# Optimization experiments

Hardware: AMD Instinct MI355X
Metric: run time of the kernel (lower is better)

The kernel has to match this reference:

```python
import jax, jax.numpy as jnp
import numpy as np

B, T_INIT, IN, H, OUT, GEN = 128, 50, 171, 1024, 171, 100


def setup_inputs() -> dict:
    key = jax.random.key(0)
    ks = jax.random.split(key, 20)
    s = 1.0 / np.sqrt(H)  # torch LSTMCell/Linear init scale

    def u(k, shape):
        return jax.random.uniform(k, shape, jnp.float32, -s, s)

    return {
        "initial_seq": jax.random.normal(ks[0], (B, T_INIT, IN), jnp.float32),
        "generate_frames_number": GEN,
        "w_ih1": u(ks[1], (4 * H, IN)), "w_hh1": u(ks[2], (4 * H, H)),
        "b_ih1": u(ks[3], (4 * H,)), "b_hh1": u(ks[4], (4 * H,)),
        "w_ih2": u(ks[5], (4 * H, H)), "w_hh2": u(ks[6], (4 * H, H)),
        "b_ih2": u(ks[7], (4 * H,)), "b_hh2": u(ks[8], (4 * H,)),
        "w_ih3": u(ks[9], (4 * H, H)), "w_hh3": u(ks[10], (4 * H, H)),
        "b_ih3": u(ks[11], (4 * H,)), "b_hh3": u(ks[12], (4 * H,)),
        "w_dec": u(ks[13], (OUT, H)), "b_dec": u(ks[14], (OUT,)),
    }


def _lstm_cell(x, h, c, w_ih, w_hh, b_ih, b_hh):
    # PyTorch LSTMCell: gates ordered (i, f, g, o)
    gates = x @ w_ih.T + b_ih + h @ w_hh.T + b_hh
    i, f, g, o = jnp.split(gates, 4, axis=-1)
    c_new = jax.nn.sigmoid(f) * c + jax.nn.sigmoid(i) * jnp.tanh(g)
    h_new = jax.nn.sigmoid(o) * jnp.tanh(c_new)
    return h_new, c_new


def reference(initial_seq, generate_frames_number,
              w_ih1, w_hh1, b_ih1, b_hh1,
              w_ih2, w_hh2, b_ih2, b_hh2,
              w_ih3, w_hh3, b_ih3, b_hh3,
              w_dec, b_dec):
    batch = initial_seq.shape[0]
    hid = w_hh1.shape[1]
    z = jnp.zeros((batch, hid), initial_seq.dtype)

    def step(carry, in_frame):
        h0, c0, h1, c1, h2, c2 = carry
        h0, c0 = _lstm_cell(in_frame, h0, c0, w_ih1, w_hh1, b_ih1, b_hh1)
        h1, c1 = _lstm_cell(h0, h1, c1, w_ih2, w_hh2, b_ih2, b_hh2)
        h2, c2 = _lstm_cell(h1, h2, c2, w_ih3, w_hh3, b_ih3, b_hh3)
        out = h2 @ w_dec.T + b_dec
        return (h0, c0, h1, c1, h2, c2), out

    # Conditioning phase: feed ground-truth frames; only states (and last out) matter.
    carry = (z, z, z, z, z, z)
    def cond_step(cs, frame):
        carry, _ = cs
        carry, out = step(carry, frame)
        return (carry, out), None
    (carry, current_frame), _ = jax.lax.scan(
        cond_step, (carry, jnp.zeros((batch, w_dec.shape[0]), initial_seq.dtype)),
        jnp.swapaxes(initial_seq, 0, 1))  # [T_init, B, IN]

    def gen_step(cs, _):
        carry, frame = cs
        carry, out = step(carry, frame)
        return (carry, out), out
    _, outs = jax.lax.scan(gen_step, (carry, current_frame), None,
                           length=generate_frames_number)
    return jnp.swapaxes(outs, 0, 1)  # [B, GEN, OUT]
```

## Files before the change

### kernel.cpp

```cpp
#include <hip/hip_runtime.h>

typedef __attribute__((ext_vector_type(8))) short short8;
typedef __attribute__((ext_vector_type(8))) _Float16 f16x8;
typedef __attribute__((ext_vector_type(4))) float f32x4;

#define GENF 100
#define TCOND 50
#define BATCH 128
#define HID 1024
#define INP 171
#define INPAD 192
#define OUTN 171
#define OUTPAD 176
#define SPLITS 4
#define TILES 64

static __device__ __forceinline__ unsigned short f2h(float f) {
  _Float16 h = (_Float16)f;
  return __builtin_bit_cast(unsigned short, h);
}
static __device__ __forceinline__ float h2f(unsigned short s) {
  return (float)__builtin_bit_cast(_Float16, s);
}
static __device__ __forceinline__ f16x8 ld8(const unsigned short* p) {
  short8 v = *reinterpret_cast<const short8*>(p);
  return __builtin_bit_cast(f16x8, v);
}
static __device__ __forceinline__ float sigm(float x) { return 1.f / (1.f + __expf(-x)); }

__global__ __launch_bounds__(256) void lstm_gemm_k(
    const unsigned short* __restrict__ xh_, const unsigned short* __restrict__ xl_,
    int ldx, int xc,
    const unsigned short* __restrict__ hh_, const unsigned short* __restrict__ hl_,
    const unsigned short* __restrict__ wH,
    int ldw, int NK,
    const float* __restrict__ bias,
    float* __restrict__ c,
    unsigned short* __restrict__ ohh, unsigned short* __restrict__ ohl,
    float* __restrict__ partials, unsigned* __restrict__ counters)
{
  __shared__ __align__(16) char smem[98304];
  const int t = threadIdx.x;
  const int lane = t & 63, wv = t >> 6;
  const int nt = blockIdx.x & (TILES - 1), sp = blockIdx.x >> 6;
  const int n0 = nt * 64 + wv * 16;
  const int nit = NK / SPLITS;
  const int beg = sp * nit;
  const int ns = nit >> 1;

  const int r_row = lane & 15, kg = lane >> 4;
  const int rslot = kg ^ (r_row & 3);
  const int srow = t >> 2;
  const size_t bcol = (size_t)(n0 + r_row) * ldw + kg * 8;

  auto stage1 = [&](char* dst, int ck) {
    const unsigned short *sh, *sl;
    int ld, k0;
    if (ck < xc) { sh = xh_; sl = xl_; ld = ldx; k0 = ck * 32; }
    else { sh = hh_; sl = hl_; ld = HID; k0 = (ck - xc) * 32; }
#pragma unroll
    for (int j = 0; j < 2; ++j) {
      int rowp = j * 64 + srow;
      int slot = (t & 3) ^ (rowp & 3);
      const unsigned short* gh = sh + (size_t)rowp * ld + k0 + slot * 8;
      const unsigned short* gl = sl + (size_t)rowp * ld + k0 + slot * 8;
      char* dh = dst + j * 4096 + wv * 1024;
      char* dl = dst + 8192 + j * 4096 + wv * 1024;
      __builtin_amdgcn_global_load_lds((const __attribute__((address_space(1))) void*)gh,
                                       (__attribute__((address_space(3))) void*)dh, 16, 0, 0);
      __builtin_amdgcn_global_load_lds((const __attribute__((address_space(1))) void*)gl,
                                       (__attribute__((address_space(3))) void*)dl, 16, 0, 0);
    }
  };

  f32x4 zz = {0.f, 0.f, 0.f, 0.f};
  f32x4 acc[8] = {zz, zz, zz, zz, zz, zz, zz, zz};

  char* bA = smem;
  char* bB = smem + 32768;
  char* bC = smem + 65536;

  stage1(bA, beg);
  stage1(bA + 16384, beg + 1);
  f16x8 b0h0 = ld8(wH + bcol + (size_t)(beg + 0) * 32);
  f16x8 b0h1 = ld8(wH + bcol + (size_t)(beg + 1) * 32);
  __builtin_amdgcn_sched_barrier(0);
  stage1(bB, beg + 2);
  stage1(bB + 16384, beg + 3);
  f16x8 b1h0 = ld8(wH + bcol + (size_t)(beg + 2) * 32);
  f16x8 b1h1 = ld8(wH + bcol + (size_t)(beg + 3) * 32);
  __builtin_amdgcn_sched_barrier(0);

  for (int i = 0; i < ns; ++i) {
    int ck = beg + 2 * i + 4;
    if (ck >= beg + nit) ck = beg;
    stage1(bC, ck);
    stage1(bC + 16384, ck + 1);
    f16x8 b2h0 = ld8(wH + bcol + (size_t)ck * 32);
    f16x8 b2h1 = ld8(wH + bcol + (size_t)(ck + 1) * 32);
    __builtin_amdgcn_sched_barrier(0);

    asm volatile("s_waitcnt vmcnt(20)" ::: "memory");
    __builtin_amdgcn_s_barrier();
    __builtin_amdgcn_sched_barrier(0);

#pragma unroll
    for (int ch = 0; ch < 2; ++ch) {
      f16x8 ah[8], al[8];
#pragma unroll
      for (int rg = 0; rg < 8; ++rg) {
        int ro = ch * 16384 + (rg * 16 + r_row) * 64 + rslot * 16;
        ah[rg] = *reinterpret_cast<const f16x8*>(bA + ro);
        al[rg] = *reinterpret_cast<const f16x8*>(bA + ro + 8192);
      }
      f16x8 BH = ch ? b0h1 : b0h0;
#pragma unroll
      for (int rg = 0; rg < 8; ++rg)
        acc[rg] = __builtin_amdgcn_mfma_f32_16x16x32_f16(ah[rg], BH, acc[rg], 0, 0, 0);
#pragma unroll
      for (int rg = 0; rg < 8; ++rg)
        acc[rg] = __builtin_amdgcn_mfma_f32_16x16x32_f16(al[rg], BH, acc[rg], 0, 0, 0);
    }
    __builtin_amdgcn_sched_barrier(0);
    __builtin_amdgcn_s_barrier();

    char* tmp = bA; bA = bB; bB = bC; bC = tmp;
    b0h0 = b1h0; b0h1 = b1h1;
    b1h0 = b2h0; b1h1 = b2h1;
  }

  {
    float* pb = partials + (size_t)sp * (BATCH * 4096);
    const int cn = n0 + r_row;
    const int mb = kg * 4;
#pragma unroll
    for (int rg = 0; rg < 8; ++rg)
#pragma unroll
      for (int r = 0; r < 4; ++r)
        pb[(size_t)(rg * 16 + mb + r) * 4096 + cn] = acc[rg][r];
  }

  __syncthreads();
  __shared__ unsigned oldv;
  if (t == 0)
    oldv = __hip_atomic_fetch_add(&counters[nt], 1u, __ATOMIC_ACQ_REL, __HIP_MEMORY_SCOPE_AGENT);
  __syncthreads();
  if (oldv != SPLITS - 1) return;

  (void)__hip_atomic_load(&counters[nt], __ATOMIC_ACQUIRE, __HIP_MEMORY_SCOPE_AGENT);
  const int fc = t & 15, fm = t >> 4;
  const int nh = nt * 16 + fc;
  const f32x4 bv = *reinterpret_cast<const f32x4*>(&bias[nh * 4]);
#pragma unroll
  for (int p = 0; p < 8; ++p) {
    int m = fm + p * 16;
    size_t gi0 = (size_t)m * 4096 + nh * 4;
    f32x4 s = *reinterpret_cast<const f32x4*>(&partials[gi0]);
#pragma unroll
    for (int q = 1; q < SPLITS; ++q)
      s += *reinterpret_cast<const f32x4*>(&partials[gi0 + (size_t)q * BATCH * 4096]);
    float gi = sigm(s[0] + bv[0]);
    float gf = sigm(s[1] + bv[1]);
    float gg = tanhf(s[2] + bv[2]);
    float go = sigm(s[3] + bv[3]);
    size_t sidx = (size_t)m * HID + nh;
    float cn2 = gf * c[sidx] + gi * gg;
    c[sidx] = cn2;
    float h = go * tanhf(cn2);
    unsigned short h16 = f2h(h);
    ohh[sidx] = h16;
    ohl[sidx] = f2h(h - h2f(h16));
  }
  __syncthreads();
  if (t == 0)
    __hip_atomic_store(&counters[nt], 0u, __ATOMIC_RELAXED, __HIP_MEMORY_SCOPE_AGENT);
}

__global__ __launch_bounds__(256) void dec_k(
    const unsigned short* __restrict__ hhi, const unsigned short* __restrict__ hlo,
    const unsigned short* __restrict__ wdh,
    const float* __restrict__ bd,
    float* __restrict__ outp,
    unsigned short* __restrict__ fxhi, unsigned short* __restrict__ fxlo)
{
  const int wave = threadIdx.x >> 6, lane = threadIdx.x & 63;
  const int n0 = ((int)blockIdx.x % 11) * 16;
  const int m0 = ((int)blockIdx.x / 11) * 16;
  const int row = lane & 15, kg = lane >> 4;
  f32x4 acc = {0.f, 0.f, 0.f, 0.f};
  const unsigned short* pah = hhi + (size_t)(m0 + row) * HID + kg * 8 + wave * 256;
  const unsigned short* pal = hlo + (size_t)(m0 + row) * HID + kg * 8 + wave * 256;
  const unsigned short* pbh = wdh + (size_t)(n0 + row) * HID + kg * 8 + wave * 256;
#pragma unroll
  for (int kk = 0; kk < 8; ++kk) {
    int off = kk * 32;
    f16x8 a1 = ld8(pah + off), a2 = ld8(pal + off);
    f16x8 b1 = ld8(pbh + off);
    acc = __builtin_amdgcn_mfma_f32_16x16x32_f16(a1, b1, acc, 0, 0, 0);
    acc = __builtin_amdgcn_mfma_f32_16x16x32_f16(a2, b1, acc, 0, 0, 0);
  }
  __shared__ f32x4 red[4][64];
  if (wave) red[wave][lane] = acc;
  __syncthreads();
  if (wave == 0) {
    acc += red[1][lane];
    acc += red[2][lane];
    acc += red[3][lane];
    const int col = lane & 15, rg = lane >> 4;
#pragma unroll
    for (int r = 0; r < 4; ++r) {
      int m = m0 + rg * 4 + r;
      int n = n0 + col;
      if (n < OUTN) {
        float v = acc[r] + bd[n];
        if (outp) outp[(size_t)m * (GENF * OUTN) + n] = v;
        unsigned short vh = f2h(v);
        fxhi[(size_t)m * INPAD + n] = vh;
        fxlo[(size_t)m * INPAD + n] = f2h(v - h2f(vh));
      }
    }
  }
}

__global__ void cvt_w_k(const float* __restrict__ src, unsigned short* __restrict__ w16,
                        int C, int Cpad, int co, int dstride)
{
  int idx = blockIdx.x * 256 + threadIdx.x;
  if (idx >= 4096 * Cpad) return;
  int r = idx / Cpad, cc = idx - r * Cpad;
  float v = (cc < C) ? src[(size_t)r * C + cc] : 0.f;
  int rp = (r & 1023) * 4 + (r >> 10);
  w16[(size_t)rp * dstride + co + cc] = f2h(v);
}

__global__ void cvt_wd_k(const float* __restrict__ src, unsigned short* __restrict__ w16,
                         int R, int C, int Rp, int Cp)
{
  int idx = blockIdx.x * 256 + threadIdx.x;
  if (idx >= Rp * Cp) return;
  int r = idx / Cp, c2 = idx - r * Cp;
  float v = (r < R && c2 < C) ? src[(size_t)r * C + c2] : 0.f;
  w16[idx] = f2h(v);
}

__global__ void bias_perm_k(const float* __restrict__ a, const float* __restrict__ b,
                            float* __restrict__ dst)
{
  int i = blockIdx.x * 256 + threadIdx.x;
  if (i < 4096) dst[(i & 1023) * 4 + (i >> 10)] = a[i] + b[i];
}

__global__ void biaspad_k(const float* __restrict__ a, float* __restrict__ dst, int n, int np)
{
  int i = blockIdx.x * 256 + threadIdx.x;
  if (i < np) dst[i] = (i < n) ? a[i] : 0.f;
}

__global__ void xcond_k(const float* __restrict__ seq, unsigned short* __restrict__ xhi,
                        unsigned short* __restrict__ xlo)
{
  int idx = blockIdx.x * 256 + threadIdx.x;
  const int total = TCOND * BATCH * INPAD;
  if (idx >= total) return;
  int t = idx / (BATCH * INPAD);
  int rem = idx - t * (BATCH * INPAD);
  int b = rem / INPAD;
  int k = rem - b * INPAD;
  float v = (k < INP) ? seq[((size_t)b * TCOND + t) * INP + k] : 0.f;
  unsigned short h = f2h(v);
  xhi[idx] = h;
  xlo[idx] = f2h(v - h2f(h));
}

extern "C" void kernel_launch(void* const* d_in, const int* in_sizes, int n_in,
                              void* d_out, int out_size, void* d_ws, size_t ws_size,
                              hipStream_t stream)
{
  (void)in_sizes; (void)n_in; (void)out_size;
  const float* seq   = (const float*)d_in[0];
  const float* w_ih1 = (const float*)d_in[2];
  const float* w_hh1 = (const float*)d_in[3];
  const float* b_ih1 = (const float*)d_in[4];
  const float* b_hh1 = (const float*)d_in[5];
  const float* w_ih2 = (const float*)d_in[6];
  const float* w_hh2 = (const float*)d_in[7];
  const float* b_ih2 = (const float*)d_in[8];
  const float* b_hh2 = (const float*)d_in[9];
  const float* w_ih3 = (const float*)d_in[10];
  const float* w_hh3 = (const float*)d_in[11];
  const float* b_ih3 = (const float*)d_in[12];
  const float* b_hh3 = (const float*)d_in[13];
  const float* w_dec = (const float*)d_in[14];
  const float* b_dec = (const float*)d_in[15];
  float* out = (float*)d_out;

  char* ws = (char*)d_ws;
  size_t off = 0;
  auto alloc = [&](size_t bytes) -> char* {
    off = (off + 255) & ~(size_t)255;
    char* p = ws + off;
    off += bytes;
    return p;
  };
  auto us = [&](size_t n) { return (unsigned short*)alloc(n * 2); };
  auto fl = [&](size_t n) { return (float*)alloc(n * 4); };

  const int K1P = 1280;
  const int K2 = 2 * HID;
  unsigned short *W1 = us((size_t)4096 * K1P);
  unsigned short *W2 = us((size_t)4096 * K2);
  unsigned short *W3 = us((size_t)4096 * K2);
  unsigned short *wd = us((size_t)OUTPAD * HID);
  float *b1 = fl(4096), *b2 = fl(4096), *b3 = fl(4096), *bd = fl(OUTPAD);
  unsigned short *xch = us((size_t)TCOND * BATCH * INPAD), *xcl = us((size_t)TCOND * BATCH * INPAD);
  float* partials = fl((size_t)SPLITS * BATCH * 4096);

  size_t state_beg = (off + 255) & ~(size_t)255;
  float *c0 = fl((size_t)BATCH * HID), *c1 = fl((size_t)BATCH * HID), *c2 = fl((size_t)BATCH * HID);
  unsigned short* Hh[3][2];
  unsigned short* Hl[3][2];
  for (int L = 0; L < 3; ++L)
    for (int p = 0; p < 2; ++p) {
      Hh[L][p] = us((size_t)BATCH * HID);
      Hl[L][p] = us((size_t)BATCH * HID);
    }
  unsigned short *fxh = us((size_t)BATCH * INPAD), *fxl = us((size_t)BATCH * INPAD);
  unsigned* counters = (unsigned*)alloc(TILES * 4);
  size_t state_end = off;

  if (off > ws_size) return;

  hipMemsetAsync(ws + state_beg, 0, state_end - state_beg, stream);
  hipMemsetAsync(W1, 0, (size_t)4096 * K1P * 2, stream);

  auto cw = [&](const float* s, unsigned short* w, int C, int Cpad, int co, int ds2) {
    int n = 4096 * Cpad;
    cvt_w_k<<<(n + 255) / 256, 256, 0, stream>>>(s, w, C, Cpad, co, ds2);
  };
  cw(w_ih1, W1, INP, INPAD, 0, K1P);
  cw(w_hh1, W1, HID, HID, INPAD, K1P);
  cw(w_ih2, W2, HID, HID, 0, K2);
  cw(w_hh2, W2, HID, HID, HID, K2);
  cw(w_ih3, W3, HID, HID, 0, K2);
  cw(w_hh3, W3, HID, HID, HID, K2);
  {
    int n = OUTPAD * HID;
    cvt_wd_k<<<(n + 255) / 256, 256, 0, stream>>>(w_dec, wd, OUTN, HID, OUTPAD, HID);
  }
  bias_perm_k<<<16, 256, 0, stream>>>(b_ih1, b_hh1, b1);
  bias_perm_k<<<16, 256, 0, stream>>>(b_ih2, b_hh2, b2);
  bias_perm_k<<<16, 256, 0, stream>>>(b_ih3, b_hh3, b3);
  biaspad_k<<<1, 256, 0, stream>>>(b_dec, bd, OUTN, OUTPAD);
  {
    int n = TCOND * BATCH * INPAD;
    xcond_k<<<(n + 255) / 256, 256, 0, stream>>>(seq, xch, xcl);
  }

  for (int s = 0; s < TCOND + GENF; ++s) {
    const unsigned short *xh, *xl;
    if (s < TCOND) {
      xh = xch + (size_t)s * BATCH * INPAD;
      xl = xcl + (size_t)s * BATCH * INPAD;
    } else {
      xh = fxh;
      xl = fxl;
    }
    int pp = s & 1, np = pp ^ 1;
    lstm_gemm_k<<<TILES * SPLITS, 256, 0, stream>>>(xh, xl, INPAD, INPAD / 32,
        Hh[0][pp], Hl[0][pp], W1, K1P, K1P / 32, b1, c0,
        Hh[0][np], Hl[0][np], partials, counters);
    lstm_gemm_k<<<TILES * SPLITS, 256, 0, stream>>>(Hh[0][np], Hl[0][np], HID, HID / 32,
        Hh[1][pp], Hl[1][pp], W2, K2, K2 / 32, b2, c1,
        Hh[1][np], Hl[1][np], partials, counters);
    lstm_gemm_k<<<TILES * SPLITS, 256, 0, stream>>>(Hh[1][np], Hl[1][np], HID, HID / 32,
        Hh[2][pp], Hl[2][pp], W3, K2, K2 / 32, b3, c2,
        Hh[2][np], Hl[2][np], partials, counters);
    if (s == TCOND - 1) {
      dec_k<<<88, 256, 0, stream>>>(Hh[2][np], Hl[2][np], wd, bd,
                                    (float*)nullptr, fxh, fxl);
    } else if (s >= TCOND) {
      dec_k<<<88, 256, 0, stream>>>(Hh[2][np], Hl[2][np], wd, bd,
                                    out + (size_t)(s - TCOND) * OUTN, fxh, fxl);
    }
  }
}
```

Before: 14.10 ms.

## Fuse all timesteps into one persistent kernel with global phase barriers

Replaces about 550 separate kernel launches (three LSTM layers plus the decoder per step) with a single persistent kernel of 256 blocks. Blocks run every step and layer in a loop and synchronize through an atomic phase counter with spin-waits. This removes launch overhead and inter-kernel gaps on the serial recurrence. The cost is a grid-wide barrier after each phase, and it relies on all 256 blocks being co-resident, otherwise it deadlocks.

```diff
diff --git a/kernel.cpp b/kernel.cpp
--- a/kernel.cpp
+++ b/kernel.cpp
@@ -14,6 +14,7 @@
 #define OUTPAD 176
 #define SPLITS 4
 #define TILES 64
+#define NBLK 256
 
 static __device__ __forceinline__ unsigned short f2h(float f) {
   _Float16 h = (_Float16)f;
@@ -28,7 +29,32 @@
 }
 static __device__ __forceinline__ float sigm(float x) { return 1.f / (1.f + __expf(-x)); }
 
-__global__ __launch_bounds__(256) void lstm_gemm_k(
+static __device__ __forceinline__ void wait_phase(unsigned* ctr, unsigned tgt) {
+  __syncthreads();
+  if (threadIdx.x == 0) {
+    while (__hip_atomic_load(ctr, __ATOMIC_RELAXED, __HIP_MEMORY_SCOPE_AGENT) < tgt)
+      __builtin_amdgcn_s_sleep(4);
+    (void)__hip_atomic_load(ctr, __ATOMIC_ACQUIRE, __HIP_MEMORY_SCOPE_AGENT);
+  }
+  __syncthreads();
+}
+
+struct Params {
+  const unsigned short* xch; const unsigned short* xcl;
+  unsigned short* fxh; unsigned short* fxl;
+  const unsigned short* wH[3];
+  const float* bias[3];
+  float* c[3];
+  unsigned short* hh[3][2]; unsigned short* hl[3][2];
+  const unsigned short* wd; const float* bd;
+  float* out;
+  float* partials;
+  unsigned* counters;
+  unsigned* phase_ctr;
+};
+
+static __device__ __forceinline__ void layer_phase(
+    char* smem, int blk,
     const unsigned short* __restrict__ xh_, const unsigned short* __restrict__ xl_,
     int ldx, int xc,
     const unsigned short* __restrict__ hh_, const unsigned short* __restrict__ hl_,
@@ -37,12 +63,12 @@
     const float* __restrict__ bias,
     float* __restrict__ c,
     unsigned short* __restrict__ ohh, unsigned short* __restrict__ ohl,
-    float* __restrict__ partials, unsigned* __restrict__ counters)
-{
-  __shared__ __align__(16) char smem[98304];
+    float* __restrict__ partials, unsigned* __restrict__ counters,
+    unsigned* __restrict__ phase_ctr)
+{
   const int t = threadIdx.x;
   const int lane = t & 63, wv = t >> 6;
-  const int nt = blockIdx.x & (TILES - 1), sp = blockIdx.x >> 6;
+  const int nt = blk & (TILES - 1), sp = blk >> 6;
   const int n0 = nt * 64 + wv * 16;
   const int nit = NK / SPLITS;
   const int beg = sp * nit;
@@ -172,34 +198,37 @@
     ohl[sidx] = f2h(h - h2f(h16));
   }
   __syncthreads();
-  if (t == 0)
+  if (t == 0) {
     __hip_atomic_store(&counters[nt], 0u, __ATOMIC_RELAXED, __HIP_MEMORY_SCOPE_AGENT);
-}
-
-__global__ __launch_bounds__(256) void dec_k(
+    __hip_atomic_fetch_add(phase_ctr, 1u, __ATOMIC_RELEASE, __HIP_MEMORY_SCOPE_AGENT);
+  }
+}
+
+static __device__ __forceinline__ void dec_phase(
+    char* smem, int blk,
     const unsigned short* __restrict__ hhi, const unsigned short* __restrict__ hlo,
-    const unsigned short* __restrict__ wdh,
-    const float* __restrict__ bd,
-    float* __restrict__ outp,
-    unsigned short* __restrict__ fxhi, unsigned short* __restrict__ fxlo)
+    const unsigned short* __restrict__ wd,
+    const float* __restrict__ bd, float* __restrict__ outp,
+    unsigned short* __restrict__ fxhi, unsigned short* __restrict__ fxlo,
+    unsigned* __restrict__ phase_ctr)
 {
   const int wave = threadIdx.x >> 6, lane = threadIdx.x & 63;
-  const int n0 = ((int)blockIdx.x % 11) * 16;
-  const int m0 = ((int)blockIdx.x / 11) * 16;
+  const int n0 = (blk % 11) * 16;
+  const int m0 = (blk / 11) * 16;
   const int row = lane & 15, kg = lane >> 4;
   f32x4 acc = {0.f, 0.f, 0.f, 0.f};
   const unsigned short* pah = hhi + (size_t)(m0 + row) * HID + kg * 8 + wave * 256;
   const unsigned short* pal = hlo + (size_t)(m0 + row) * HID + kg * 8 + wave * 256;
-  const unsigned short* pbh = wdh + (size_t)(n0 + row) * HID + kg * 8 + wave * 256;
+  const unsigned short* pbh = wd + (size_t)(n0 + row) * HID + kg * 8 + wave * 256;
 #pragma unroll
   for (int kk = 0; kk < 8; ++kk) {
-    int off = kk * 32;
-    f16x8 a1 = ld8(pah + off), a2 = ld8(pal + off);
-    f16x8 b1 = ld8(pbh + off);
+    int off2 = kk * 32;
+    f16x8 a1 = ld8(pah + off2), a2 = ld8(pal + off2);
+    f16x8 b1 = ld8(pbh + off2);
     acc = __builtin_amdgcn_mfma_f32_16x16x32_f16(a1, b1, acc, 0, 0, 0);
     acc = __builtin_amdgcn_mfma_f32_16x16x32_f16(a2, b1, acc, 0, 0, 0);
   }
-  __shared__ f32x4 red[4][64];
+  f32x4 (*red)[64] = (f32x4(*)[64])smem;
   if (wave) red[wave][lane] = acc;
   __syncthreads();
   if (wave == 0) {
@@ -218,6 +247,49 @@
         fxhi[(size_t)m * INPAD + n] = vh;
         fxlo[(size_t)m * INPAD + n] = f2h(v - h2f(vh));
       }
+    }
+  }
+  __syncthreads();
+  if (threadIdx.x == 0)
+    __hip_atomic_fetch_add(phase_ctr, 1u, __ATOMIC_RELEASE, __HIP_MEMORY_SCOPE_AGENT);
+}
+
+__global__ __launch_bounds__(256) void lstm_persist_k(Params p) {
+  __shared__ __align__(16) char smem[98304];
+  const int blk = blockIdx.x;
+  unsigned tgt = 0;
+  for (int s = 0; s < TCOND + GENF; ++s) {
+    const int pp = s & 1, np = pp ^ 1;
+    for (int L = 0; L < 3; ++L) {
+      const unsigned short *xh, *xl;
+      int ldx, xc, ldw, NK;
+      if (L == 0) {
+        if (s < TCOND) {
+          xh = p.xch + (size_t)s * BATCH * INPAD;
+          xl = p.xcl + (size_t)s * BATCH * INPAD;
+        } else {
+          xh = p.fxh;
+          xl = p.fxl;
+        }
+        ldx = INPAD; xc = INPAD / 32; ldw = 1280; NK = 40;
+      } else {
+        xh = p.hh[L - 1][np]; xl = p.hl[L - 1][np];
+        ldx = HID; xc = HID / 32; ldw = 2 * HID; NK = 64;
+      }
+      layer_phase(smem, blk, xh, xl, ldx, xc, p.hh[L][pp], p.hl[L][pp],
+                  p.wH[L], ldw, NK, p.bias[L], p.c[L],
+                  p.hh[L][np], p.hl[L][np], p.partials, p.counters, p.phase_ctr);
+      tgt += TILES;
+      wait_phase(p.phase_ctr, tgt);
+    }
+    if (s >= TCOND - 1) {
+      if (blk < 88) {
+        float* outp = (s >= TCOND) ? p.out + (size_t)(s - TCOND) * OUTN : (float*)0;
+        dec_phase(smem, blk, p.hh[2][np], p.hl[2][np], p.wd, p.bd,
+                  outp, p.fxh, p.fxl, p.phase_ctr);
+      }
+      tgt += 88;
+      wait_phase(p.phase_ctr, tgt);
     }
   }
 }
@@ -326,6 +398,7 @@
     }
   unsigned short *fxh = us((size_t)BATCH * INPAD), *fxl = us((size_t)BATCH * INPAD);
   unsigned* counters = (unsigned*)alloc(TILES * 4);
+  unsigned* phase_ctr = (unsigned*)alloc(4);
   size_t state_end = off;
 
   if (off > ws_size) return;
@@ -356,31 +429,20 @@
     xcond_k<<<(n + 255) / 256, 256, 0, stream>>>(seq, xch, xcl);
   }
 
-  for (int s = 0; s < TCOND + GENF; ++s) {
-    const unsigned short *xh, *xl;
-    if (s < TCOND) {
-      xh = xch + (size_t)s * BATCH * INPAD;
-      xl = xcl + (size_t)s * BATCH * INPAD;
-    } else {
-      xh = fxh;
-      xl = fxl;
-    }
-    int pp = s & 1, np = pp ^ 1;
-    lstm_gemm_k<<<TILES * SPLITS, 256, 0, stream>>>(xh, xl, INPAD, INPAD / 32,
-        Hh[0][pp], Hl[0][pp], W1, K1P, K1P / 32, b1, c0,
-        Hh[0][np], Hl[0][np], partials, counters);
-    lstm_gemm_k<<<TILES * SPLITS, 256, 0, stream>>>(Hh[0][np], Hl[0][np], HID, HID / 32,
-        Hh[1][pp], Hl[1][pp], W2, K2, K2 / 32, b2, c1,
-        Hh[1][np], Hl[1][np], partials, counters);
-    lstm_gemm_k<<<TILES * SPLITS, 256, 0, stream>>>(Hh[1][np], Hl[1][np], HID, HID / 32,
-        Hh[2][pp], Hl[2][pp], W3, K2, K2 / 32, b3, c2,
-        Hh[2][np], Hl[2][np], partials, counters);
-    if (s == TCOND - 1) {
-      dec_k<<<88, 256, 0, stream>>>(Hh[2][np], Hl[2][np], wd, bd,
-                                    (float*)nullptr, fxh, fxl);
-    } else if (s >= TCOND) {
-      dec_k<<<88, 256, 0, stream>>>(Hh[2][np], Hl[2][np], wd, bd,
-                                    out + (size_t)(s - TCOND) * OUTN, fxh, fxl);
-    }
-  }
-}
+  Params P;
+  P.xch = xch; P.xcl = xcl; P.fxh = fxh; P.fxl = fxl;
+  P.wH[0] = W1; P.wH[1] = W2; P.wH[2] = W3;
+  P.bias[0] = b1; P.bias[1] = b2; P.bias[2] = b3;
+  P.c[0] = c0; P.c[1] = c1; P.c[2] = c2;
+  for (int L = 0; L < 3; ++L)
+    for (int p2 = 0; p2 < 2; ++p2) {
+      P.hh[L][p2] = Hh[L][p2];
+      P.hl[L][p2] = Hl[L][p2];
+    }
+  P.wd = wd; P.bd = bd;
+  P.out = out;
+  P.partials = partials;
+  P.counters = counters;
+  P.phase_ctr = phase_ctr;
+  lstm_persist_k<<<NBLK, 256, 0, stream>>>(P);
+}
```

New measurement: 18.89 ms. 1.34x slower.

## Drop split-K partials; each block computes full K for 16 gate columns

Applied to the files above, without the earlier changes.

Replaces the split-K scheme (64 N-tiles × 4 K-splits, fp32 partials written to global memory, atomic counter, last-block reduction) with 256 blocks that each own 16 gate columns across the full K range and all 128 batch rows. The LSTM cell epilogue reads the accumulators through shared memory instead of global partials, which removes the partial-sum traffic and the atomic synchronisation. In exchange, each block runs a K loop four times longer with fewer MFMAs per staged A tile, and every block re-stages the whole activation matrix into LDS, so LDS and L2 pressure rise. Padding allocations are added after the layer-0 state buffers, apparently so the K-loop prefetch wrap does not read past the buffer.

```diff
diff --git a/kernel.cpp b/kernel.cpp
--- a/kernel.cpp
+++ b/kernel.cpp
@@ -12,8 +12,6 @@
 #define INPAD 192
 #define OUTN 171
 #define OUTPAD 176
-#define SPLITS 4
-#define TILES 64
 
 static __device__ __forceinline__ unsigned short f2h(float f) {
   _Float16 h = (_Float16)f;
@@ -36,22 +34,19 @@
     int ldw, int NK,
     const float* __restrict__ bias,
     float* __restrict__ c,
-    unsigned short* __restrict__ ohh, unsigned short* __restrict__ ohl,
-    float* __restrict__ partials, unsigned* __restrict__ counters)
+    unsigned short* __restrict__ ohh, unsigned short* __restrict__ ohl)
 {
   __shared__ __align__(16) char smem[98304];
   const int t = threadIdx.x;
   const int lane = t & 63, wv = t >> 6;
-  const int nt = blockIdx.x & (TILES - 1), sp = blockIdx.x >> 6;
-  const int n0 = nt * 64 + wv * 16;
-  const int nit = NK / SPLITS;
-  const int beg = sp * nit;
-  const int ns = nit >> 1;
+  const int blk = blockIdx.x;
+  const int ns = NK >> 1;
 
   const int r_row = lane & 15, kg = lane >> 4;
   const int rslot = kg ^ (r_row & 3);
   const int srow = t >> 2;
-  const size_t bcol = (size_t)(n0 + r_row) * ldw + kg * 8;
+  const size_t bcol = (size_t)(blk * 16 + r_row) * ldw + kg * 8;
+  const int arow = wv * 32;
 
   auto stage1 = [&](char* dst, int ck) {
     const unsigned short *sh, *sl;
@@ -74,26 +69,26 @@
   };
 
   f32x4 zz = {0.f, 0.f, 0.f, 0.f};
-  f32x4 acc[8] = {zz, zz, zz, zz, zz, zz, zz, zz};
+  f32x4 acc0 = zz, acc1 = zz;
 
   char* bA = smem;
   char* bB = smem + 32768;
   char* bC = smem + 65536;
 
-  stage1(bA, beg);
-  stage1(bA + 16384, beg + 1);
-  f16x8 b0h0 = ld8(wH + bcol + (size_t)(beg + 0) * 32);
-  f16x8 b0h1 = ld8(wH + bcol + (size_t)(beg + 1) * 32);
+  stage1(bA, 0);
+  stage1(bA + 16384, 1);
+  f16x8 b0h0 = ld8(wH + bcol + (size_t)0 * 32);
+  f16x8 b0h1 = ld8(wH + bcol + (size_t)1 * 32);
   __builtin_amdgcn_sched_barrier(0);
-  stage1(bB, beg + 2);
-  stage1(bB + 16384, beg + 3);
-  f16x8 b1h0 = ld8(wH + bcol + (size_t)(beg + 2) * 32);
-  f16x8 b1h1 = ld8(wH + bcol + (size_t)(beg + 3) * 32);
+  stage1(bB, 2);
+  stage1(bB + 16384, 3);
+  f16x8 b1h0 = ld8(wH + bcol + (size_t)2 * 32);
+  f16x8 b1h1 = ld8(wH + bcol + (size_t)3 * 32);
   __builtin_amdgcn_sched_barrier(0);
 
   for (int i = 0; i < ns; ++i) {
-    int ck = beg + 2 * i + 4;
-    if (ck >= beg + nit) ck = beg;
+    int ck = 2 * i + 4;
+    if (ck >= NK) ck = 0;
     stage1(bC, ck);
     stage1(bC + 16384, ck + 1);
     f16x8 b2h0 = ld8(wH + bcol + (size_t)ck * 32);
@@ -106,20 +101,16 @@
 
 #pragma unroll
     for (int ch = 0; ch < 2; ++ch) {
-      f16x8 ah[8], al[8];
-#pragma unroll
-      for (int rg = 0; rg < 8; ++rg) {
-        int ro = ch * 16384 + (rg * 16 + r_row) * 64 + rslot * 16;
-        ah[rg] = *reinterpret_cast<const f16x8*>(bA + ro);
-        al[rg] = *reinterpret_cast<const f16x8*>(bA + ro + 8192);
-      }
+      int ro = ch * 16384 + (arow + r_row) * 64 + rslot * 16;
+      f16x8 ah0 = *reinterpret_cast<const f16x8*>(bA + ro);
+      f16x8 al0 = *reinterpret_cast<const f16x8*>(bA + ro + 8192);
+      f16x8 ah1 = *reinterpret_cast<const f16x8*>(bA + ro + 1024);
+      f16x8 al1 = *reinterpret_cast<const f16x8*>(bA + ro + 1024 + 8192);
       f16x8 BH = ch ? b0h1 : b0h0;
-#pragma unroll
-      for (int rg = 0; rg < 8; ++rg)
-        acc[rg] = __builtin_amdgcn_mfma_f32_16x16x32_f16(ah[rg], BH, acc[rg], 0, 0, 0);
-#pragma unroll
-      for (int rg = 0; rg < 8; ++rg)
-        acc[rg] = __builtin_amdgcn_mfma_f32_16x16x32_f16(al[rg], BH, acc[rg], 0, 0, 0);
+      acc0 = __builtin_amdgcn_mfma_f32_16x16x32_f16(ah0, BH, acc0, 0, 0, 0);
+      acc0 = __builtin_amdgcn_mfma_f32_16x16x32_f16(al0, BH, acc0, 0, 0, 0);
+      acc1 = __builtin_amdgcn_mfma_f32_16x16x32_f16(ah1, BH, acc1, 0, 0, 0);
+      acc1 = __builtin_amdgcn_mfma_f32_16x16x32_f16(al1, BH, acc1, 0, 0, 0);
     }
     __builtin_amdgcn_sched_barrier(0);
     __builtin_amdgcn_s_barrier();
@@ -129,41 +120,29 @@
     b1h0 = b2h0; b1h1 = b2h1;
   }
 
-  {
-    float* pb = partials + (size_t)sp * (BATCH * 4096);
-    const int cn = n0 + r_row;
-    const int mb = kg * 4;
-#pragma unroll
-    for (int rg = 0; rg < 8; ++rg)
-#pragma unroll
-      for (int r = 0; r < 4; ++r)
-        pb[(size_t)(rg * 16 + mb + r) * 4096 + cn] = acc[rg][r];
-  }
-
+  asm volatile("s_waitcnt vmcnt(0)" ::: "memory");
+  __builtin_amdgcn_s_barrier();
+
+  float* gb = reinterpret_cast<float*>(smem) + wv * 512;
+#pragma unroll
+  for (int r = 0; r < 4; ++r) {
+    gb[(kg * 4 + r) * 16 + r_row] = acc0[r];
+    gb[(16 + kg * 4 + r) * 16 + r_row] = acc1[r];
+  }
   __syncthreads();
-  __shared__ unsigned oldv;
-  if (t == 0)
-    oldv = __hip_atomic_fetch_add(&counters[nt], 1u, __ATOMIC_ACQ_REL, __HIP_MEMORY_SCOPE_AGENT);
-  __syncthreads();
-  if (oldv != SPLITS - 1) return;
-
-  (void)__hip_atomic_load(&counters[nt], __ATOMIC_ACQUIRE, __HIP_MEMORY_SCOPE_AGENT);
-  const int fc = t & 15, fm = t >> 4;
-  const int nh = nt * 16 + fc;
-  const f32x4 bv = *reinterpret_cast<const f32x4*>(&bias[nh * 4]);
-#pragma unroll
-  for (int p = 0; p < 8; ++p) {
-    int m = fm + p * 16;
-    size_t gi0 = (size_t)m * 4096 + nh * 4;
-    f32x4 s = *reinterpret_cast<const f32x4*>(&partials[gi0]);
-#pragma unroll
-    for (int q = 1; q < SPLITS; ++q)
-      s += *reinterpret_cast<const f32x4*>(&partials[gi0 + (size_t)q * BATCH * 4096]);
-    float gi = sigm(s[0] + bv[0]);
-    float gf = sigm(s[1] + bv[1]);
-    float gg = tanhf(s[2] + bv[2]);
-    float go = sigm(s[3] + bv[3]);
-    size_t sidx = (size_t)m * HID + nh;
+
+#pragma unroll
+  for (int e = 0; e < 2; ++e) {
+    int o = e * 64 + lane;
+    int rl = o >> 2, c0 = o & 3;
+    f32x4 g4 = *reinterpret_cast<const f32x4*>(gb + rl * 16 + c0 * 4);
+    int nh_g = blk * 4 + c0;
+    f32x4 bv = *reinterpret_cast<const f32x4*>(&bias[nh_g * 4]);
+    float gi = sigm(g4[0] + bv[0]);
+    float gf = sigm(g4[1] + bv[1]);
+    float gg = tanhf(g4[2] + bv[2]);
+    float go = sigm(g4[3] + bv[3]);
+    size_t sidx = (size_t)(arow + rl) * HID + nh_g;
     float cn2 = gf * c[sidx] + gi * gg;
     c[sidx] = cn2;
     float h = go * tanhf(cn2);
@@ -171,9 +150,6 @@
     ohh[sidx] = h16;
     ohl[sidx] = f2h(h - h2f(h16));
   }
-  __syncthreads();
-  if (t == 0)
-    __hip_atomic_store(&counters[nt], 0u, __ATOMIC_RELAXED, __HIP_MEMORY_SCOPE_AGENT);
 }
 
 __global__ __launch_bounds__(256) void dec_k(
@@ -313,7 +289,6 @@
   unsigned short *wd = us((size_t)OUTPAD * HID);
   float *b1 = fl(4096), *b2 = fl(4096), *b3 = fl(4096), *bd = fl(OUTPAD);
   unsigned short *xch = us((size_t)TCOND * BATCH * INPAD), *xcl = us((size_t)TCOND * BATCH * INPAD);
-  float* partials = fl((size_t)SPLITS * BATCH * 4096);
 
   size_t state_beg = (off + 255) & ~(size_t)255;
   float *c0 = fl((size_t)BATCH * HID), *c1 = fl((size_t)BATCH * HID), *c2 = fl((size_t)BATCH * HID);
@@ -322,10 +297,11 @@
   for (int L = 0; L < 3; ++L)
     for (int p = 0; p < 2; ++p) {
       Hh[L][p] = us((size_t)BATCH * HID);
+      if (L == 0) alloc(4096);
       Hl[L][p] = us((size_t)BATCH * HID);
+      if (L == 0) alloc(4096);
     }
   unsigned short *fxh = us((size_t)BATCH * INPAD), *fxl = us((size_t)BATCH * INPAD);
-  unsigned* counters = (unsigned*)alloc(TILES * 4);
   size_t state_end = off;
 
   if (off > ws_size) return;
@@ -366,15 +342,12 @@
       xl = fxl;
     }
     int pp = s & 1, np = pp ^ 1;
-    lstm_gemm_k<<<TILES * SPLITS, 256, 0, stream>>>(xh, xl, INPAD, INPAD / 32,
-        Hh[0][pp], Hl[0][pp], W1, K1P, K1P / 32, b1, c0,
-        Hh[0][np], Hl[0][np], partials, counters);
-    lstm_gemm_k<<<TILES * SPLITS, 256, 0, stream>>>(Hh[0][np], Hl[0][np], HID, HID / 32,
-        Hh[1][pp], Hl[1][pp], W2, K2, K2 / 32, b2, c1,
-        Hh[1][np], Hl[1][np], partials, counters);
-    lstm_gemm_k<<<TILES * SPLITS, 256, 0, stream>>>(Hh[1][np], Hl[1][np], HID, HID / 32,
-        Hh[2][pp], Hl[2][pp], W3, K2, K2 / 32, b3, c2,
-        Hh[2][np], Hl[2][np], partials, counters);
+    lstm_gemm_k<<<256, 256, 0, stream>>>(xh, xl, INPAD, INPAD / 32,
+        Hh[0][pp], Hl[0][pp], W1, K1P, K1P / 32, b1, c0, Hh[0][np], Hl[0][np]);
+    lstm_gemm_k<<<256, 256, 0, stream>>>(Hh[0][np], Hl[0][np], HID, HID / 32,
+        Hh[1][pp], Hl[1][pp], W2, K2, K2 / 32, b2, c1, Hh[1][np], Hl[1][np]);
+    lstm_gemm_k<<<256, 256, 0, stream>>>(Hh[1][np], Hl[1][np], HID, HID / 32,
+        Hh[2][pp], Hl[2][pp], W3, K2, K2 / 32, b3, c2, Hh[2][np], Hl[2][np]);
     if (s == TCOND - 1) {
       dec_k<<<88, 256, 0, stream>>>(Hh[2][np], Hl[2][np], wd, bd,
                                     (float*)nullptr, fxh, fxl);
```

After: 17.99 ms. 1.28x slower.

## Fold decoder into layer-1 weights and overlap recurrent GEMMs across layers

Applied to the files above, without the earlier changes.

During generation the decoder output feeds layer 1, so the code precomputes W_ih1·W_dec and a matching bias. Layer 1 then consumes h2 directly, and the per-step decoder launch is removed. The recurrent h@W_hh products of layers 2 and 3 depend only on previous-step states, so they run in the same launch as layer 1. That leaves each layer's dependent kernel with only the input half of its K dimension. All decoder outputs come from one batched GEMM over a stored h2 history at the end. The fused weight is rounded to fp16, which changes numerics, and the history buffer adds memory traffic.

```diff
diff --git a/kernel.cpp b/kernel.cpp
--- a/kernel.cpp
+++ b/kernel.cpp
@@ -12,8 +12,8 @@
 #define INPAD 192
 #define OUTN 171
 #define OUTPAD 176
-#define SPLITS 4
 #define TILES 64
+#define PSTR ((size_t)BATCH * 4096)
 
 static __device__ __forceinline__ unsigned short f2h(float f) {
   _Float16 h = (_Float16)f;
@@ -28,24 +28,18 @@
 }
 static __device__ __forceinline__ float sigm(float x) { return 1.f / (1.f + __expf(-x)); }
 
-__global__ __launch_bounds__(256) void lstm_gemm_k(
+static __device__ __forceinline__ void core_gemm(
+    char* smem, int nt,
     const unsigned short* __restrict__ xh_, const unsigned short* __restrict__ xl_,
     int ldx, int xc,
     const unsigned short* __restrict__ hh_, const unsigned short* __restrict__ hl_,
-    const unsigned short* __restrict__ wH,
-    int ldw, int NK,
-    const float* __restrict__ bias,
-    float* __restrict__ c,
-    unsigned short* __restrict__ ohh, unsigned short* __restrict__ ohl,
-    float* __restrict__ partials, unsigned* __restrict__ counters)
-{
-  __shared__ __align__(16) char smem[98304];
+    const unsigned short* __restrict__ wH, int ldw, int nkr,
+    int beg, int nit,
+    float* __restrict__ pslot)
+{
   const int t = threadIdx.x;
   const int lane = t & 63, wv = t >> 6;
-  const int nt = blockIdx.x & (TILES - 1), sp = blockIdx.x >> 6;
   const int n0 = nt * 64 + wv * 16;
-  const int nit = NK / SPLITS;
-  const int beg = sp * nit;
   const int ns = nit >> 1;
 
   const int r_row = lane & 15, kg = lane >> 4;
@@ -54,6 +48,7 @@
   const size_t bcol = (size_t)(n0 + r_row) * ldw + kg * 8;
 
   auto stage1 = [&](char* dst, int ck) {
+    if (ck >= nkr) ck = 0;
     const unsigned short *sh, *sl;
     int ld, k0;
     if (ck < xc) { sh = xh_; sl = xl_; ld = ldx; k0 = ck * 32; }
@@ -130,24 +125,32 @@
   }
 
   {
-    float* pb = partials + (size_t)sp * (BATCH * 4096);
     const int cn = n0 + r_row;
     const int mb = kg * 4;
 #pragma unroll
     for (int rg = 0; rg < 8; ++rg)
 #pragma unroll
       for (int r = 0; r < 4; ++r)
-        pb[(size_t)(rg * 16 + mb + r) * 4096 + cn] = acc[rg][r];
-  }
-
+        pslot[(size_t)(rg * 16 + mb + r) * 4096 + cn] = acc[rg][r];
+  }
+}
+
+static __device__ __forceinline__ void fin_cell(
+    int nt, int splits, unsigned* __restrict__ cnt,
+    const float* __restrict__ pbase, int nslots,
+    const float* __restrict__ bias, float* __restrict__ c,
+    unsigned short* __restrict__ ohh, unsigned short* __restrict__ ohl,
+    unsigned short* __restrict__ histh, unsigned short* __restrict__ histl)
+{
+  const int t = threadIdx.x;
   __syncthreads();
   __shared__ unsigned oldv;
   if (t == 0)
-    oldv = __hip_atomic_fetch_add(&counters[nt], 1u, __ATOMIC_ACQ_REL, __HIP_MEMORY_SCOPE_AGENT);
+    oldv = __hip_atomic_fetch_add(&cnt[nt], 1u, __ATOMIC_ACQ_REL, __HIP_MEMORY_SCOPE_AGENT);
   __syncthreads();
-  if (oldv != SPLITS - 1) return;
-
-  (void)__hip_atomic_load(&counters[nt], __ATOMIC_ACQUIRE, __HIP_MEMORY_SCOPE_AGENT);
+  if (oldv != splits - 1) return;
+
+  (void)__hip_atomic_load(&cnt[nt], __ATOMIC_ACQUIRE, __HIP_MEMORY_SCOPE_AGENT);
   const int fc = t & 15, fm = t >> 4;
   const int nh = nt * 16 + fc;
   const f32x4 bv = *reinterpret_cast<const f32x4*>(&bias[nh * 4]);
@@ -155,10 +158,9 @@
   for (int p = 0; p < 8; ++p) {
     int m = fm + p * 16;
     size_t gi0 = (size_t)m * 4096 + nh * 4;
-    f32x4 s = *reinterpret_cast<const f32x4*>(&partials[gi0]);
-#pragma unroll
-    for (int q = 1; q < SPLITS; ++q)
-      s += *reinterpret_cast<const f32x4*>(&partials[gi0 + (size_t)q * BATCH * 4096]);
+    f32x4 s = *reinterpret_cast<const f32x4*>(&pbase[gi0]);
+    for (int q = 1; q < nslots; ++q)
+      s += *reinterpret_cast<const f32x4*>(&pbase[gi0 + (size_t)q * PSTR]);
     float gi = sigm(s[0] + bv[0]);
     float gf = sigm(s[1] + bv[1]);
     float gg = tanhf(s[2] + bv[2]);
@@ -168,28 +170,74 @@
     c[sidx] = cn2;
     float h = go * tanhf(cn2);
     unsigned short h16 = f2h(h);
+    unsigned short l16 = f2h(h - h2f(h16));
     ohh[sidx] = h16;
-    ohl[sidx] = f2h(h - h2f(h16));
+    ohl[sidx] = l16;
+    if (histh) { histh[sidx] = h16; histl[sidx] = l16; }
   }
   __syncthreads();
   if (t == 0)
-    __hip_atomic_store(&counters[nt], 0u, __ATOMIC_RELAXED, __HIP_MEMORY_SCOPE_AGENT);
-}
-
-__global__ __launch_bounds__(256) void dec_k(
-    const unsigned short* __restrict__ hhi, const unsigned short* __restrict__ hlo,
-    const unsigned short* __restrict__ wdh,
-    const float* __restrict__ bd,
-    float* __restrict__ outp,
-    unsigned short* __restrict__ fxhi, unsigned short* __restrict__ fxlo)
+    __hip_atomic_store(&cnt[nt], 0u, __ATOMIC_RELAXED, __HIP_MEMORY_SCOPE_AGENT);
+}
+
+struct AP {
+  const unsigned short *x1h, *x1l; int ldx1, xc1;
+  const unsigned short *h1h, *h1l;
+  const unsigned short* W1; int ldw1, NK1, nkr1;
+  float* p1; unsigned* cnt1; const float* b1; float* c0;
+  unsigned short *o1h, *o1l;
+  const unsigned short *a2h, *a2l; const unsigned short* W2h_; float* p2;
+  const unsigned short *a3h, *a3l; const unsigned short* W3h_; float* p3;
+};
+
+__global__ __launch_bounds__(256) void phaseA_k(AP p) {
+  __shared__ __align__(16) char smem[98304];
+  const int blk = blockIdx.x;
+  if (blk < 128) {
+    int nt = blk & 63, sp = blk >> 6;
+    int nit = p.NK1 >> 1;
+    core_gemm(smem, nt, p.x1h, p.x1l, p.ldx1, p.xc1, p.h1h, p.h1l,
+              p.W1, p.ldw1, p.nkr1, sp * nit, nit, p.p1 + sp * PSTR);
+    fin_cell(nt, 2, p.cnt1, p.p1, 2, p.b1, p.c0, p.o1h, p.o1l,
+             (unsigned short*)0, (unsigned short*)0);
+  } else if (blk < 192) {
+    int nt = blk - 128;
+    core_gemm(smem, nt, p.a2h, p.a2l, HID, 32, p.a2h, p.a2l,
+              p.W2h_, HID, 32, 0, 32, p.p2 + 4 * PSTR);
+  } else {
+    int nt = blk - 192;
+    core_gemm(smem, nt, p.a3h, p.a3l, HID, 32, p.a3h, p.a3l,
+              p.W3h_, HID, 32, 0, 32, p.p3 + 4 * PSTR);
+  }
+}
+
+struct XP {
+  const unsigned short *ah, *al;
+  const unsigned short* Wx;
+  float* pb; unsigned* cnt; const float* bias; float* c;
+  unsigned short *ohh, *ohl, *histh, *histl;
+};
+
+__global__ __launch_bounds__(256) void phaseX_k(XP p) {
+  __shared__ __align__(16) char smem[98304];
+  const int nt = blockIdx.x & 63, sp = blockIdx.x >> 6;
+  core_gemm(smem, nt, p.ah, p.al, HID, 32, p.ah, p.al,
+            p.Wx, HID, 32, sp * 8, 8, p.pb + sp * PSTR);
+  fin_cell(nt, 4, p.cnt, p.pb, 5, p.bias, p.c, p.ohh, p.ohl, p.histh, p.histl);
+}
+
+__global__ __launch_bounds__(256) void decb_k(
+    const unsigned short* __restrict__ histh, const unsigned short* __restrict__ histl,
+    const unsigned short* __restrict__ wdh, const float* __restrict__ bd,
+    float* __restrict__ outp)
 {
   const int wave = threadIdx.x >> 6, lane = threadIdx.x & 63;
   const int n0 = ((int)blockIdx.x % 11) * 16;
   const int m0 = ((int)blockIdx.x / 11) * 16;
   const int row = lane & 15, kg = lane >> 4;
   f32x4 acc = {0.f, 0.f, 0.f, 0.f};
-  const unsigned short* pah = hhi + (size_t)(m0 + row) * HID + kg * 8 + wave * 256;
-  const unsigned short* pal = hlo + (size_t)(m0 + row) * HID + kg * 8 + wave * 256;
+  const unsigned short* pah = histh + (size_t)(m0 + row) * HID + kg * 8 + wave * 256;
+  const unsigned short* pal = histl + (size_t)(m0 + row) * HID + kg * 8 + wave * 256;
   const unsigned short* pbh = wdh + (size_t)(n0 + row) * HID + kg * 8 + wave * 256;
 #pragma unroll
   for (int kk = 0; kk < 8; ++kk) {
@@ -212,11 +260,8 @@
       int m = m0 + rg * 4 + r;
       int n = n0 + col;
       if (n < OUTN) {
-        float v = acc[r] + bd[n];
-        if (outp) outp[(size_t)m * (GENF * OUTN) + n] = v;
-        unsigned short vh = f2h(v);
-        fxhi[(size_t)m * INPAD + n] = vh;
-        fxlo[(size_t)m * INPAD + n] = f2h(v - h2f(vh));
+        int tt = m >> 7, b = m & 127;
+        outp[(size_t)b * (GENF * OUTN) + (size_t)tt * OUTN + n] = acc[r] + bd[n];
       }
     }
   }
@@ -233,14 +278,63 @@
   w16[(size_t)rp * dstride + co + cc] = f2h(v);
 }
 
-__global__ void cvt_wd_k(const float* __restrict__ src, unsigned short* __restrict__ w16,
-                         int R, int C, int Rp, int Cp)
+__global__ void cvt_plain_k(const float* __restrict__ src, unsigned short* __restrict__ w16,
+                            int R, int C, int Rp, int Cp)
 {
   int idx = blockIdx.x * 256 + threadIdx.x;
   if (idx >= Rp * Cp) return;
   int r = idx / Cp, c2 = idx - r * Cp;
   float v = (r < R && c2 < C) ? src[(size_t)r * C + c2] : 0.f;
   w16[idx] = f2h(v);
+}
+
+__global__ void cvt_wdt_k(const float* __restrict__ wdec, unsigned short* __restrict__ wdt)
+{
+  int idx = blockIdx.x * 256 + threadIdx.x;
+  if (idx >= 1024 * 192) return;
+  int k = idx / 192, j = idx - k * 192;
+  float v = (j < OUTN) ? wdec[(size_t)j * HID + k] : 0.f;
+  wdt[idx] = f2h(v);
+}
+
+__global__ __launch_bounds__(256) void weff_k(
+    const unsigned short* __restrict__ wih, const unsigned short* __restrict__ wdt,
+    unsigned short* __restrict__ W1g)
+{
+  const int wave = threadIdx.x >> 6, lane = threadIdx.x & 63;
+  const int tile = blockIdx.x * 4 + wave;
+  const int m0 = (tile >> 6) * 16;
+  const int n0 = (tile & 63) * 16;
+  const int row = lane & 15, kg = lane >> 4;
+  f32x4 acc = {0.f, 0.f, 0.f, 0.f};
+  const unsigned short* pa = wih + (size_t)(m0 + row) * 192 + kg * 8;
+  const unsigned short* pb = wdt + (size_t)(n0 + row) * 192 + kg * 8;
+#pragma unroll
+  for (int kk = 0; kk < 6; ++kk) {
+    int off = kk * 32;
+    f16x8 a = ld8(pa + off);
+    f16x8 b = ld8(pb + off);
+    acc = __builtin_amdgcn_mfma_f32_16x16x32_f16(a, b, acc, 0, 0, 0);
+  }
+  const int col = lane & 15, rg = lane >> 4;
+#pragma unroll
+  for (int r = 0; r < 4; ++r) {
+    int i = m0 + rg * 4 + r;
+    int k2 = n0 + col;
+    int rp = (i & 1023) * 4 + (i >> 10);
+    W1g[(size_t)rp * 2048 + k2] = f2h(acc[r]);
+  }
+}
+
+__global__ void beff_k(const float* __restrict__ wih1, const float* __restrict__ bih,
+                       const float* __restrict__ bhh, const float* __restrict__ bdec,
+                       float* __restrict__ dst)
+{
+  int i = blockIdx.x * 256 + threadIdx.x;
+  if (i >= 4096) return;
+  float a = bih[i] + bhh[i];
+  for (int j = 0; j < OUTN; ++j) a += wih1[(size_t)i * OUTN + j] * bdec[j];
+  dst[(i & 1023) * 4 + (i >> 10)] = a;
 }
 
 __global__ void bias_perm_k(const float* __restrict__ a, const float* __restrict__ b,
@@ -305,15 +399,23 @@
   auto us = [&](size_t n) { return (unsigned short*)alloc(n * 2); };
   auto fl = [&](size_t n) { return (float*)alloc(n * 4); };
 
-  const int K1P = 1280;
-  const int K2 = 2 * HID;
-  unsigned short *W1 = us((size_t)4096 * K1P);
-  unsigned short *W2 = us((size_t)4096 * K2);
-  unsigned short *W3 = us((size_t)4096 * K2);
-  unsigned short *wd = us((size_t)OUTPAD * HID);
-  float *b1 = fl(4096), *b2 = fl(4096), *b3 = fl(4096), *bd = fl(OUTPAD);
+  const int K1C = 1536;
+  unsigned short* W1c = us((size_t)4096 * K1C);
+  unsigned short* W1g = us((size_t)4096 * 2048);
+  unsigned short* W2x = us((size_t)4096 * HID);
+  unsigned short* W2h = us((size_t)4096 * HID);
+  unsigned short* W3x = us((size_t)4096 * HID);
+  unsigned short* W3h = us((size_t)4096 * HID);
+  unsigned short* wd = us((size_t)OUTPAD * HID);
+  unsigned short* wih1f = us((size_t)4096 * 192);
+  unsigned short* wdt = us((size_t)1024 * 192);
+  float *b1c = fl(4096), *beff = fl(4096), *b2 = fl(4096), *b3 = fl(4096), *bd = fl(OUTPAD);
   unsigned short *xch = us((size_t)TCOND * BATCH * INPAD), *xcl = us((size_t)TCOND * BATCH * INPAD);
-  float* partials = fl((size_t)SPLITS * BATCH * 4096);
+  float* pL1 = fl(2 * PSTR);
+  float* pL2 = fl(5 * PSTR);
+  float* pL3 = fl(5 * PSTR);
+  unsigned short* histh = us((size_t)GENF * BATCH * HID);
+  unsigned short* histl = us((size_t)GENF * BATCH * HID);
 
   size_t state_beg = (off + 255) & ~(size_t)255;
   float *c0 = fl((size_t)BATCH * HID), *c1 = fl((size_t)BATCH * HID), *c2 = fl((size_t)BATCH * HID);
@@ -324,63 +426,75 @@
       Hh[L][p] = us((size_t)BATCH * HID);
       Hl[L][p] = us((size_t)BATCH * HID);
     }
-  unsigned short *fxh = us((size_t)BATCH * INPAD), *fxl = us((size_t)BATCH * INPAD);
-  unsigned* counters = (unsigned*)alloc(TILES * 4);
+  unsigned* counters = (unsigned*)alloc(192 * 4);
   size_t state_end = off;
 
   if (off > ws_size) return;
 
   hipMemsetAsync(ws + state_beg, 0, state_end - state_beg, stream);
-  hipMemsetAsync(W1, 0, (size_t)4096 * K1P * 2, stream);
-
-  auto cw = [&](const float* s, unsigned short* w, int C, int Cpad, int co, int ds2) {
-    int n = 4096 * Cpad;
-    cvt_w_k<<<(n + 255) / 256, 256, 0, stream>>>(s, w, C, Cpad, co, ds2);
-  };
-  cw(w_ih1, W1, INP, INPAD, 0, K1P);
-  cw(w_hh1, W1, HID, HID, INPAD, K1P);
-  cw(w_ih2, W2, HID, HID, 0, K2);
-  cw(w_hh2, W2, HID, HID, HID, K2);
-  cw(w_ih3, W3, HID, HID, 0, K2);
-  cw(w_hh3, W3, HID, HID, HID, K2);
-  {
-    int n = OUTPAD * HID;
-    cvt_wd_k<<<(n + 255) / 256, 256, 0, stream>>>(w_dec, wd, OUTN, HID, OUTPAD, HID);
-  }
-  bias_perm_k<<<16, 256, 0, stream>>>(b_ih1, b_hh1, b1);
+  hipMemsetAsync(W1c, 0, (size_t)4096 * K1C * 2, stream);
+
+  cvt_w_k<<<(4096 * INPAD + 255) / 256, 256, 0, stream>>>(w_ih1, W1c, INP, INPAD, 0, K1C);
+  cvt_w_k<<<(4096 * 1024 + 255) / 256, 256, 0, stream>>>(w_hh1, W1c, HID, HID, INPAD, K1C);
+  cvt_w_k<<<(4096 * 1024 + 255) / 256, 256, 0, stream>>>(w_hh1, W1g, HID, HID, 1024, 2048);
+  cvt_w_k<<<(4096 * 1024 + 255) / 256, 256, 0, stream>>>(w_ih2, W2x, HID, HID, 0, HID);
+  cvt_w_k<<<(4096 * 1024 + 255) / 256, 256, 0, stream>>>(w_hh2, W2h, HID, HID, 0, HID);
+  cvt_w_k<<<(4096 * 1024 + 255) / 256, 256, 0, stream>>>(w_ih3, W3x, HID, HID, 0, HID);
+  cvt_w_k<<<(4096 * 1024 + 255) / 256, 256, 0, stream>>>(w_hh3, W3h, HID, HID, 0, HID);
+  cvt_plain_k<<<(OUTPAD * HID + 255) / 256, 256, 0, stream>>>(w_dec, wd, OUTN, HID, OUTPAD, HID);
+  cvt_plain_k<<<(4096 * 192 + 255) / 256, 256, 0, stream>>>(w_ih1, wih1f, 4096, INP, 4096, 192);
+  cvt_wdt_k<<<(1024 * 192 + 255) / 256, 256, 0, stream>>>(w_dec, wdt);
+  weff_k<<<4096, 256, 0, stream>>>(wih1f, wdt, W1g);
+  beff_k<<<16, 256, 0, stream>>>(w_ih1, b_ih1, b_hh1, b_dec, beff);
+  bias_perm_k<<<16, 256, 0, stream>>>(b_ih1, b_hh1, b1c);
   bias_perm_k<<<16, 256, 0, stream>>>(b_ih2, b_hh2, b2);
   bias_perm_k<<<16, 256, 0, stream>>>(b_ih3, b_hh3, b3);
   biaspad_k<<<1, 256, 0, stream>>>(b_dec, bd, OUTN, OUTPAD);
-  {
-    int n = TCOND * BATCH * INPAD;
-    xcond_k<<<(n + 255) / 256, 256, 0, stream>>>(seq, xch, xcl);
-  }
+  xcond_k<<<(TCOND * BATCH * INPAD + 255) / 256, 256, 0, stream>>>(seq, xch, xcl);
 
   for (int s = 0; s < TCOND + GENF; ++s) {
-    const unsigned short *xh, *xl;
+    const int pp = s & 1, np = pp ^ 1;
+    AP a;
     if (s < TCOND) {
-      xh = xch + (size_t)s * BATCH * INPAD;
-      xl = xcl + (size_t)s * BATCH * INPAD;
+      a.x1h = xch + (size_t)s * BATCH * INPAD;
+      a.x1l = xcl + (size_t)s * BATCH * INPAD;
+      a.ldx1 = INPAD; a.xc1 = INPAD / 32;
+      a.W1 = W1c; a.ldw1 = K1C; a.NK1 = K1C / 32; a.nkr1 = 38;
+      a.b1 = b1c;
     } else {
-      xh = fxh;
-      xl = fxl;
+      a.x1h = Hh[2][pp]; a.x1l = Hl[2][pp];
+      a.ldx1 = HID; a.xc1 = 32;
+      a.W1 = W1g; a.ldw1 = 2048; a.NK1 = 64; a.nkr1 = 64;
+      a.b1 = beff;
     }
-    int pp = s & 1, np = pp ^ 1;
-    lstm_gemm_k<<<TILES * SPLITS, 256, 0, stream>>>(xh, xl, INPAD, INPAD / 32,
-        Hh[0][pp], Hl[0][pp], W1, K1P, K1P / 32, b1, c0,
-        Hh[0][np], Hl[0][np], partials, counters);
-    lstm_gemm_k<<<TILES * SPLITS, 256, 0, stream>>>(Hh[0][np], Hl[0][np], HID, HID / 32,
-        Hh[1][pp], Hl[1][pp], W2, K2, K2 / 32, b2, c1,
-        Hh[1][np], Hl[1][np], partials, counters);
-    lstm_gemm_k<<<TILES * SPLITS, 256, 0, stream>>>(Hh[1][np], Hl[1][np], HID, HID / 32,
-        Hh[2][pp], Hl[2][pp], W3, K2, K2 / 32, b3, c2,
-        Hh[2][np], Hl[2][np], partials, counters);
-    if (s == TCOND - 1) {
-      dec_k<<<88, 256, 0, stream>>>(Hh[2][np], Hl[2][np], wd, bd,
-                                    (float*)nullptr, fxh, fxl);
-    } else if (s >= TCOND) {
-      dec_k<<<88, 256, 0, stream>>>(Hh[2][np], Hl[2][np], wd, bd,
-                                    out + (size_t)(s - TCOND) * OUTN, fxh, fxl);
+    a.h1h = Hh[0][pp]; a.h1l = Hl[0][pp];
+    a.p1 = pL1; a.cnt1 = counters; a.c0 = c0;
+    a.o1h = Hh[0][np]; a.o1l = Hl[0][np];
+    a.a2h = Hh[1][pp]; a.a2l = Hl[1][pp]; a.W2h_ = W2h; a.p2 = pL2;
+    a.a3h = Hh[2][pp]; a.a3l = Hl[2][pp]; a.W3h_ = W3h; a.p3 = pL3;
+    phaseA_k<<<256, 256, 0, stream>>>(a);
+
+    XP b;
+    b.ah = Hh[0][np]; b.al = Hl[0][np];
+    b.Wx = W2x; b.pb = pL2; b.cnt = counters + 64;
+    b.bias = b2; b.c = c1;
+    b.ohh = Hh[1][np]; b.ohl = Hl[1][np];
+    b.histh = (unsigned short*)0; b.histl = (unsigned short*)0;
+    phaseX_k<<<256, 256, 0, stream>>>(b);
+
+    XP cx;
+    cx.ah = Hh[1][np]; cx.al = Hl[1][np];
+    cx.Wx = W3x; cx.pb = pL3; cx.cnt = counters + 128;
+    cx.bias = b3; cx.c = c2;
+    cx.ohh = Hh[2][np]; cx.ohl = Hl[2][np];
+    if (s >= TCOND) {
+      cx.histh = histh + (size_t)(s - TCOND) * BATCH * HID;
+      cx.histl = histl + (size_t)(s - TCOND) * BATCH * HID;
+    } else {
+      cx.histh = (unsigned short*)0; cx.histl = (unsigned short*)0;
     }
-  }
-}
+    phaseX_k<<<256, 256, 0, stream>>>(cx);
+  }
+
+  decb_k<<<(GENF * BATCH / 16) * 11, 256, 0, stream>>>(histh, histl, wd, bd, out);
+}
```

Result: slower. 14.57 ms (+3.3%).
